# Optimization experiments

Measured on AMD Instinct MI355X. Metric: run time of the kernel, lower is better.

Reference implementation:

```python
import jax, jax.numpy as jnp
import numpy as np

N_NODES = 50000
N_EDGES = 800000
N_GRAPHS = 64
HEADS = 8
HID = 16
D = HEADS * HID  # 128
N_CLASSES = 10
NEG_SLOPE = 0.2
N_LAYERS = 5


def setup_inputs() -> dict:
    key = jax.random.key(0)
    ks = jax.random.split(key, 12)
    x = jax.random.normal(ks[0], (N_NODES, D), dtype=jnp.float32)
    edge_index = jax.random.randint(ks[1], (2, N_EDGES), 0, N_NODES, dtype=jnp.int32)
    batch = jnp.sort(jax.random.randint(ks[2], (N_NODES,), 0, N_GRAPHS, dtype=jnp.int32))
    s = 1.0 / np.sqrt(D)
    # all 5 GATv2 layers share the same shapes (in = 8*hidden = 128); stack on axis 0
    Wl = jax.random.normal(ks[3], (N_LAYERS, D, D), dtype=jnp.float32) * s
    bl = jnp.zeros((N_LAYERS, D), dtype=jnp.float32)
    Wr = jax.random.normal(ks[4], (N_LAYERS, D, D), dtype=jnp.float32) * s
    br = jnp.zeros((N_LAYERS, D), dtype=jnp.float32)
    att = jax.random.normal(ks[5], (N_LAYERS, HEADS, HID), dtype=jnp.float32) * (1.0 / np.sqrt(HID))
    bias = jnp.zeros((N_LAYERS, D), dtype=jnp.float32)
    Wout = jax.random.normal(ks[6], (D, N_CLASSES), dtype=jnp.float32) * s
    bout = jnp.zeros((N_CLASSES,), dtype=jnp.float32)
    return {"x": x, "edge_index": edge_index, "batch": batch,
            "Wl": Wl, "bl": bl, "Wr": Wr, "br": br, "att": att, "bias": bias,
            "Wout": Wout, "bout": bout}


def gatv2_layer(x, src, dst, Wl, bl, Wr, br, att, bias):
    # x: [N, D_in]; returns [N, HEADS*HID]
    n = x.shape[0]
    xl = (x @ Wl + bl).reshape(n, HEADS, HID)   # source/message transform
    xr = (x @ Wr + br).reshape(n, HEADS, HID)   # target transform
    # GATv2 attention: att . leaky_relu(xl_j + xr_i) per edge, per head
    e = jax.nn.leaky_relu(xl[src] + xr[dst], NEG_SLOPE)          # [E, H, C]
    logits = jnp.einsum('ehc,hc->eh', e, att)                    # [E, H]
    # segment-softmax over incoming edges of each dst node
    m = jax.ops.segment_max(logits, dst, num_segments=n)         # [N, H]
    p = jnp.exp(logits - m[dst])
    denom = jax.ops.segment_sum(p, dst, num_segments=n)          # [N, H]
    alpha = p / denom[dst]                                       # [E, H]
    msg = xl[src] * alpha[:, :, None]                            # [E, H, C]
    out = jax.ops.segment_sum(msg, dst, num_segments=n)
    return out.reshape(n, HEADS * HID) + bias


def reference(x, edge_index, batch, Wl, bl, Wr, br, att, bias, Wout, bout):
    n = x.shape[0]
    # GATv2Conv(add_self_loops=True): append self loops to the edge list
    loops = jnp.arange(n, dtype=edge_index.dtype)
    src = jnp.concatenate([edge_index[0], loops])
    dst = jnp.concatenate([edge_index[1], loops])
    h = x
    for l in range(N_LAYERS):
        h = gatv2_layer(h, src, dst, Wl[l], bl[l], Wr[l], br[l], att[l], bias[l])
        h = jax.nn.elu(h)
    # global mean pool over graphs
    sums = jax.ops.segment_sum(h, batch, num_segments=N_GRAPHS)       # [G, D]
    counts = jax.ops.segment_sum(jnp.ones((n,), h.dtype), batch, num_segments=N_GRAPHS)
    pooled = sums / jnp.maximum(counts, 1.0)[:, None]
    logits = pooled @ Wout + bout
    return jax.nn.log_softmax(logits, axis=1)
```

## Files before the change

kernel.cpp:

```cpp
#include <hip/hip_runtime.h>
#include <hip/hip_bf16.h>
#include <math.h>

#define DD 128
#define HEADS 8
#define HID 16
#define NEG_SLOPE 0.2f
#define N_LAYERS 5
#define N_GRAPHS 64
#define N_CLASSES 10
#define NBINS 256
#define BIN_CAP 8192

typedef __bf16 bf16x8 __attribute__((ext_vector_type(8)));
typedef float f32x4 __attribute__((ext_vector_type(4)));

__device__ __forceinline__ float bflo(unsigned u) { return __uint_as_float(u << 16); }
__device__ __forceinline__ float bfhi(unsigned u) { return __uint_as_float(u & 0xffff0000u); }
__device__ __forceinline__ float bf1(unsigned short us) { return __uint_as_float(((unsigned)us) << 16); }
__device__ __forceinline__ unsigned short f2bf(float f) {
    unsigned u = __float_as_uint(f);
    u += 0x7fffu + ((u >> 16) & 1u);
    return (unsigned short)(u >> 16);
}
__device__ __forceinline__ unsigned pack2bf(float a, float b) {
    return (unsigned)f2bf(a) | ((unsigned)f2bf(b) << 16);
}

#define WCNT (N_LAYERS * 4 * 16 * 64)


__global__ void k_setup(const float* __restrict__ x, unsigned* __restrict__ xb,
                        const float* __restrict__ Wl, const float* __restrict__ Wr,
                        unsigned short* __restrict__ wB,
                        float* __restrict__ pooled, float* __restrict__ counts, int n2) {
    int id = blockIdx.x * 256 + threadIdx.x;
    if (id < n2) {
        float2 v = *(const float2*)(x + 2 * (size_t)id);
        xb[id] = pack2bf(v.x, v.y);
        return;
    }
    id -= n2;
    if (id < WCNT) {
        int lane = id & 63;
        int ntg  = (id >> 6) & 15;
        int ks   = (id >> 10) & 3;
        int l    = id >> 12;
        int q = lane >> 4, r = lane & 15;
        int n = ntg * 16 + r;
        const float* W = ((n < DD) ? Wl : Wr) + (size_t)l * DD * DD;
        int nn = n & (DD - 1);
        size_t off = (size_t)l * (4 * 16 * 64 * 8) + ((size_t)(ks * 16 + ntg) * 64 + lane) * 8;
        for (int j = 0; j < 8; ++j) {
            int k = ks * 32 + q * 8 + j;
            wB[off + j] = f2bf(W[(size_t)k * DD + nn]);
        }
        return;
    }
    id -= WCNT;
    if (id < N_GRAPHS * DD) { pooled[id] = 0.f; return; }
    id -= N_GRAPHS * DD;
    if (id < N_GRAPHS) counts[id] = 0.f;
}


__global__ __launch_bounds__(256) void k_bin_cnt(const int* __restrict__ ei,
        int* __restrict__ cnt, int n_edges, int n_total, int chunk,
        unsigned long long bin_mul) {
    __shared__ int hist[NBINS];
    int tid = threadIdx.x;
    hist[tid] = 0;
    __syncthreads();
    int beg = blockIdx.x * chunk;
    int end = beg + chunk; if (end > n_total) end = n_total;
    for (int e = beg + tid; e < end; e += 256) {
        int d = (e < n_edges) ? ei[n_edges + e] : (e - n_edges);
        int b = (int)(((unsigned long long)(unsigned)d * bin_mul) >> 32);
        atomicAdd(&hist[b], 1);
    }
    __syncthreads();
    cnt[tid * 256 + blockIdx.x] = hist[tid];
}

__global__ __launch_bounds__(256) void k_bin_scan(int* __restrict__ cnt, int* __restrict__ btot) {
    __shared__ int wsum[4];
    int b = blockIdx.x, t = threadIdx.x, wv = t >> 6, ln = t & 63;
    int v = cnt[b * 256 + t];
    int x = v;
#pragma unroll
    for (int ofs = 1; ofs < 64; ofs <<= 1) {
        int tt = __shfl_up(x, ofs);
        if (ln >= ofs) x += tt;
    }
    if (ln == 63) wsum[wv] = x;
    __syncthreads();
    int off = 0;
    for (int k = 0; k < wv; k++) off += wsum[k];
    int incl = off + x;
    cnt[b * 256 + t] = incl - v;
    if (t == 255) btot[b] = incl;
}

__global__ __launch_bounds__(256) void k_tot_scan(const int* __restrict__ btot,
        int* __restrict__ bin_start, int* __restrict__ row_ptr, int n_nodes) {
    __shared__ int wsum[4];
    int t = threadIdx.x, wv = t >> 6, ln = t & 63;
    int v = btot[t];
    int x = v;
#pragma unroll
    for (int ofs = 1; ofs < 64; ofs <<= 1) {
        int tt = __shfl_up(x, ofs);
        if (ln >= ofs) x += tt;
    }
    if (ln == 63) wsum[wv] = x;
    __syncthreads();
    int off = 0;
    for (int k = 0; k < wv; k++) off += wsum[k];
    int incl = off + x;
    bin_start[t] = incl - v;
    if (t == 255) { bin_start[256] = incl; row_ptr[n_nodes] = incl; }
}

__global__ __launch_bounds__(256) void k_bin_scatter(const int* __restrict__ ei,
        const int* __restrict__ cnt, const int* __restrict__ bin_start,
        unsigned* __restrict__ binned, int n_edges, int n_total, int chunk,
        unsigned long long bin_mul) {
    __shared__ int cur[NBINS];
    int tid = threadIdx.x;
    cur[tid] = bin_start[tid] + cnt[tid * 256 + blockIdx.x];
    __syncthreads();
    int beg = blockIdx.x * chunk;
    int end = beg + chunk; if (end > n_total) end = n_total;
    for (int e = beg + tid; e < end; e += 256) {
        int s, d;
        if (e < n_edges) { s = ei[e]; d = ei[n_edges + e]; }
        else { s = d = e - n_edges; }
        int b = (int)(((unsigned long long)(unsigned)d * bin_mul) >> 32);
        int pos = atomicAdd(&cur[b], 1);
        binned[pos] = (unsigned)s | ((unsigned)d << 16);
    }
}

__global__ __launch_bounds__(256) void k_bin_csr(const unsigned* __restrict__ binned,
        const int* __restrict__ bin_start, int* __restrict__ csr_src,
        int* __restrict__ row_ptr, int n_nodes, unsigned long long bin_mul) {
    __shared__ int sbuf[BIN_CAP];
    __shared__ int ldeg[256];
    __shared__ int wsum[4];
    int b = blockIdx.x, t = threadIdx.x, wv = t >> 6, ln = t & 63;
    int lo = (int)(((((unsigned long long)b) << 32) + bin_mul - 1) / bin_mul);
    int hi = (int)(((((unsigned long long)(b + 1)) << 32) + bin_mul - 1) / bin_mul);
    if (hi > n_nodes) hi = n_nodes;
    int estart = bin_start[b], eend = bin_start[b + 1];
    int ne = eend - estart;
    ldeg[t] = 0;
    __syncthreads();
    for (int k = t; k < ne; k += 256) {
        unsigned v = binned[estart + k];
        atomicAdd(&ldeg[(int)(v >> 16) - lo], 1);
    }
    __syncthreads();
    int vdeg = ldeg[t];
    int x = vdeg;
#pragma unroll
    for (int ofs = 1; ofs < 64; ofs <<= 1) {
        int tt = __shfl_up(x, ofs);
        if (ln >= ofs) x += tt;
    }
    if (ln == 63) wsum[wv] = x;
    __syncthreads();
    int off = 0;
    for (int k = 0; k < wv; k++) off += wsum[k];
    int excl = off + x - vdeg;
    if (lo + t < hi) row_ptr[lo + t] = estart + excl;
    ldeg[t] = excl;
    __syncthreads();
    for (int k = t; k < ne; k += 256) {
        unsigned v = binned[estart + k];
        int pos = atomicAdd(&ldeg[(int)(v >> 16) - lo], 1);
        sbuf[pos] = (int)(v & 0xffffu);
    }
    __syncthreads();
    for (int k = t; k < ne; k += 256)
        csr_src[estart + k] = sbuf[k];
}


__global__ __launch_bounds__(256) void k_gemm_mfma(
    const unsigned short* __restrict__ in, const unsigned short* __restrict__ wB,
    const float* __restrict__ bl, const float* __restrict__ br,
    unsigned short* __restrict__ xl, unsigned short* __restrict__ xr, int n_nodes) {
    int w = threadIdx.x >> 6;
    int lane = threadIdx.x & 63;
    int q = lane >> 4, r = lane & 15;
    int blk = blockIdx.x;

    f32x4 acc[4][4] = {};
#pragma unroll
    for (int ks = 0; ks < 4; ++ks) {
        bf16x8 bh[4];
#pragma unroll
        for (int nt = 0; nt < 4; ++nt) {
            int ntg = w * 4 + nt;
            bh[nt] = *(const bf16x8*)(wB + ((size_t)(ks * 16 + ntg) * 64 + lane) * 8);
        }
        bf16x8 ah[4];
#pragma unroll
        for (int mt = 0; mt < 4; ++mt) {
            int node = blk * 64 + mt * 16 + r;
            if (node >= n_nodes) node = n_nodes - 1;
            ah[mt] = *(const bf16x8*)(in + (size_t)node * DD + ks * 32 + q * 8);
        }
#pragma unroll
        for (int mt = 0; mt < 4; ++mt)
#pragma unroll
            for (int nt = 0; nt < 4; ++nt)
                acc[mt][nt] = __builtin_amdgcn_mfma_f32_16x16x32_bf16(ah[mt], bh[nt], acc[mt][nt], 0, 0, 0);
    }
#pragma unroll
    for (int nt = 0; nt < 4; ++nt) {
        int col = w * 64 + nt * 16 + r;
        float bv = (col < DD) ? bl[col] : br[col - DD];
        unsigned short* dstbase = (col < DD) ? (xl + col) : (xr + (col - DD));
#pragma unroll
        for (int mt = 0; mt < 4; ++mt)
#pragma unroll
            for (int reg = 0; reg < 4; ++reg) {
                int node = blk * 64 + mt * 16 + q * 4 + reg;
                if (node < n_nodes)
                    dstbase[(size_t)node * DD] = f2bf(acc[mt][nt][reg] + bv);
            }
    }
}


__global__ __launch_bounds__(256) void k_node_agg(
    const unsigned short* __restrict__ xl, const unsigned short* __restrict__ xr,
    const int* __restrict__ row_ptr, const int* __restrict__ csr_src,
    const float* __restrict__ att, const float* __restrict__ bias,
    unsigned short* __restrict__ h_out, int n_nodes) {
    int wave = threadIdx.x >> 6;
    int lane = threadIdx.x & 63;
    int node = blockIdx.x * 4 + wave;
    if (node >= n_nodes) return;
    int grp = lane >> 4, sl = lane & 15;
    int beg = row_ptr[node], end = row_ptr[node + 1];

    uint4 xru = *(const uint4*)(xr + (size_t)node * DD + sl * 8);
    float xr0 = bflo(xru.x), xr1 = bfhi(xru.x), xr2 = bflo(xru.y), xr3 = bfhi(xru.y);
    float xr4 = bflo(xru.z), xr5 = bfhi(xru.z), xr6 = bflo(xru.w), xr7 = bfhi(xru.w);
    float4 at0 = *(const float4*)(att + sl * 8);
    float4 at1 = *(const float4*)(att + sl * 8 + 4);

    float l = 0.f;
    float a0 = 0.f, a1 = 0.f, a2 = 0.f, a3 = 0.f, a4 = 0.f, a5 = 0.f, a6 = 0.f, a7 = 0.f;

    int t0 = beg + grp;
    uint4 xu = make_uint4(0u, 0u, 0u, 0u);
    int sidx = 0;
    if (t0 < end) {
        int s = csr_src[t0];
        xu = *(const uint4*)(xl + (size_t)s * DD + sl * 8);
    }
    if (t0 + 4 < end) sidx = csr_src[t0 + 4];

    for (int t = t0; t < end; t += 4) {
        uint4 cur = xu;
        int snew = 0;
        if (t + 8 < end) snew = csr_src[t + 8];
        if (t + 4 < end) xu = *(const uint4*)(xl + (size_t)sidx * DD + sl * 8);
        sidx = snew;

        float x0 = bflo(cur.x), x1 = bfhi(cur.x), x2 = bflo(cur.y), x3 = bfhi(cur.y);
        float x4 = bflo(cur.z), x5 = bfhi(cur.z), x6 = bflo(cur.w), x7 = bfhi(cur.w);
        float v0 = x0 + xr0; v0 = v0 > 0.f ? v0 : NEG_SLOPE * v0;
        float v1 = x1 + xr1; v1 = v1 > 0.f ? v1 : NEG_SLOPE * v1;
        float v2 = x2 + xr2; v2 = v2 > 0.f ? v2 : NEG_SLOPE * v2;
        float v3 = x3 + xr3; v3 = v3 > 0.f ? v3 : NEG_SLOPE * v3;
        float v4 = x4 + xr4; v4 = v4 > 0.f ? v4 : NEG_SLOPE * v4;
        float v5 = x5 + xr5; v5 = v5 > 0.f ? v5 : NEG_SLOPE * v5;
        float v6 = x6 + xr6; v6 = v6 > 0.f ? v6 : NEG_SLOPE * v6;
        float v7 = x7 + xr7; v7 = v7 > 0.f ? v7 : NEG_SLOPE * v7;
        float lg = at0.x * v0 + at0.y * v1 + at0.z * v2 + at0.w * v3 +
                   at1.x * v4 + at1.y * v5 + at1.z * v6 + at1.w * v7;
        lg += __shfl_xor(lg, 1);
        float p = __expf(lg);
        l += p;
        a0 += p * x0; a1 += p * x1; a2 += p * x2; a3 += p * x3;
        a4 += p * x4; a5 += p * x5; a6 += p * x6; a7 += p * x7;
    }
    l  += __shfl_xor(l, 16);  l  += __shfl_xor(l, 32);
    a0 += __shfl_xor(a0, 16); a0 += __shfl_xor(a0, 32);
    a1 += __shfl_xor(a1, 16); a1 += __shfl_xor(a1, 32);
    a2 += __shfl_xor(a2, 16); a2 += __shfl_xor(a2, 32);
    a3 += __shfl_xor(a3, 16); a3 += __shfl_xor(a3, 32);
    a4 += __shfl_xor(a4, 16); a4 += __shfl_xor(a4, 32);
    a5 += __shfl_xor(a5, 16); a5 += __shfl_xor(a5, 32);
    a6 += __shfl_xor(a6, 16); a6 += __shfl_xor(a6, 32);
    a7 += __shfl_xor(a7, 16); a7 += __shfl_xor(a7, 32);

    if (grp == 0) {
        float4 bv0 = *(const float4*)(bias + sl * 8);
        float4 bv1 = *(const float4*)(bias + sl * 8 + 4);
        float rl = 1.f / l;
        float o0 = a0 * rl + bv0.x; o0 = o0 > 0.f ? o0 : __expf(o0) - 1.f;
        float o1 = a1 * rl + bv0.y; o1 = o1 > 0.f ? o1 : __expf(o1) - 1.f;
        float o2 = a2 * rl + bv0.z; o2 = o2 > 0.f ? o2 : __expf(o2) - 1.f;
        float o3 = a3 * rl + bv0.w; o3 = o3 > 0.f ? o3 : __expf(o3) - 1.f;
        float o4 = a4 * rl + bv1.x; o4 = o4 > 0.f ? o4 : __expf(o4) - 1.f;
        float o5 = a5 * rl + bv1.y; o5 = o5 > 0.f ? o5 : __expf(o5) - 1.f;
        float o6 = a6 * rl + bv1.z; o6 = o6 > 0.f ? o6 : __expf(o6) - 1.f;
        float o7 = a7 * rl + bv1.w; o7 = o7 > 0.f ? o7 : __expf(o7) - 1.f;
        uint4 o;
        o.x = pack2bf(o0, o1); o.y = pack2bf(o2, o3);
        o.z = pack2bf(o4, o5); o.w = pack2bf(o6, o7);
        *(uint4*)(h_out + (size_t)node * DD + sl * 8) = o;
    }
}


__global__ void k_pool2(const unsigned short* __restrict__ h, const int* __restrict__ batch,
                        float* __restrict__ pooled, float* __restrict__ counts,
                        int n_nodes, int chunk) {
    int c = threadIdx.x;
    int beg = blockIdx.x * chunk;
    if (beg >= n_nodes) return;
    int end = beg + chunk; if (end > n_nodes) end = n_nodes;
    int cur = batch[beg];
    float acc = 0.f; int cnt = 0;
    for (int node = beg; node < end; ++node) {
        int g = batch[node];
        if (g != cur) {
            atomicAdd(&pooled[cur * DD + c], acc);
            if (c == 0) atomicAdd(&counts[cur], (float)cnt);
            acc = 0.f; cnt = 0; cur = g;
        }
        acc += bf1(h[(size_t)node * DD + c]);
        cnt++;
    }
    atomicAdd(&pooled[cur * DD + c], acc);
    if (c == 0) atomicAdd(&counts[cur], (float)cnt);
}

__global__ void k_final(const float* __restrict__ pooled, const float* __restrict__ counts,
                        const float* __restrict__ Wout, const float* __restrict__ bout,
                        float* __restrict__ out) {
    __shared__ float slog[N_GRAPHS * N_CLASSES];
    int t = threadIdx.x;
    int g = t / N_CLASSES, c = t % N_CLASSES;
    float cnt = fmaxf(counts[g], 1.f);
    float acc = bout[c];
    for (int k = 0; k < DD; k++)
        acc += (pooled[g * DD + k] / cnt) * Wout[k * N_CLASSES + c];
    slog[t] = acc;
    __syncthreads();
    float mx = -INFINITY;
    for (int j = 0; j < N_CLASSES; j++) mx = fmaxf(mx, slog[g * N_CLASSES + j]);
    float se = 0.f;
    for (int j = 0; j < N_CLASSES; j++) se += __expf(slog[g * N_CLASSES + j] - mx);
    out[t] = acc - mx - __logf(se);
}

extern "C" void kernel_launch(void* const* d_in, const int* in_sizes, int n_in,
                              void* d_out, int out_size, void* d_ws, size_t ws_size,
                              hipStream_t stream) {
    const float* x     = (const float*)d_in[0];
    const int*   ei    = (const int*)d_in[1];
    const int*   batch = (const int*)d_in[2];
    const float* Wl    = (const float*)d_in[3];
    const float* bl    = (const float*)d_in[4];
    const float* Wr    = (const float*)d_in[5];
    const float* br    = (const float*)d_in[6];
    const float* att   = (const float*)d_in[7];
    const float* bias  = (const float*)d_in[8];
    const float* Wout  = (const float*)d_in[9];
    const float* bout  = (const float*)d_in[10];
    float* out = (float*)d_out;

    int n_nodes = in_sizes[0] / DD;
    int n_edges = in_sizes[1] / 2;
    int n_total = n_edges + n_nodes;
    int ND = n_nodes * DD;

    const int WPL = 4 * 16 * 64 * 8;
    unsigned long long bin_mul = (((unsigned long long)NBINS) << 32) / (unsigned)n_nodes;

    unsigned short* hb  = (unsigned short*)d_ws;
    unsigned short* xb  = hb + (size_t)ND;
    unsigned short* xlb = xb + (size_t)ND;
    unsigned short* xrb = xlb + (size_t)ND;
    unsigned short* wB  = xrb + (size_t)ND;
    int*      cnt       = (int*)(wB + (size_t)N_LAYERS * WPL);
    int*      btot      = cnt + NBINS * 256;
    int*      bin_start = btot + NBINS;
    unsigned* binned    = (unsigned*)(bin_start + NBINS + 1);
    int*      csr_src   = (int*)(binned + n_total);
    int*      row_ptr   = csr_src + n_total;
    float*    pooled    = (float*)(row_ptr + n_nodes + 1);
    float*    counts    = pooled + N_GRAPHS * DD;

    dim3 b256(256);
    int gGemm = (n_nodes + 63) / 64;
    int gAgg  = (n_nodes + 3) / 4;
    int chunk = (n_total + 255) / 256;
    int poolBlocks = 1024;
    int poolChunk = (n_nodes + poolBlocks - 1) / poolBlocks;

    int n2 = ND / 2;
    int setupTotal = n2 + WCNT + N_GRAPHS * DD + N_GRAPHS;
    k_setup<<<(setupTotal + 255) / 256, b256, 0, stream>>>(x, (unsigned*)xb, Wl, Wr, wB,
                                                           pooled, counts, n2);
    k_bin_cnt<<<256, b256, 0, stream>>>(ei, cnt, n_edges, n_total, chunk, bin_mul);
    k_bin_scan<<<NBINS, b256, 0, stream>>>(cnt, btot);
    k_tot_scan<<<1, b256, 0, stream>>>(btot, bin_start, row_ptr, n_nodes);
    k_bin_scatter<<<256, b256, 0, stream>>>(ei, cnt, bin_start, binned, n_edges, n_total,
                                            chunk, bin_mul);
    k_bin_csr<<<NBINS, b256, 0, stream>>>(binned, bin_start, csr_src, row_ptr, n_nodes, bin_mul);

    for (int l = 0; l < N_LAYERS; l++) {
        const float* bl_l   = bl   + (size_t)l * DD;
        const float* br_l   = br   + (size_t)l * DD;
        const float* att_l  = att  + (size_t)l * HEADS * HID;
        const float* bias_l = bias + (size_t)l * DD;
        const unsigned short* in = (l == 0) ? xb : hb;

        k_gemm_mfma<<<gGemm, b256, 0, stream>>>(in, wB + (size_t)l * WPL, bl_l, br_l,
                                                xlb, xrb, n_nodes);
        k_node_agg<<<gAgg, b256, 0, stream>>>(xlb, xrb, row_ptr, csr_src, att_l, bias_l, hb, n_nodes);
    }

    k_pool2<<<poolBlocks, dim3(128), 0, stream>>>(hb, batch, pooled, counts, n_nodes, poolChunk);
    k_final<<<1, dim3(N_GRAPHS * N_CLASSES), 0, stream>>>(pooled, counts, Wout, bout, out);
}
```

Measured before the change: 498.3 us.

## Fuse CSR build and pooling stages into persistent kernels with grid barriers

Merges setup, binning count, scans, scatter and CSR build into one 256-block kernel that separates phases with atomic-counter grid barriers, and merges pooling with the final classifier the same way. This cuts the per-launch overhead and inter-kernel gaps of roughly eight small launches. The leaky-relu also becomes a branchless fmaxf. The cost is a memset for the barrier counters. Correctness also depends on all 256 blocks being co-resident and on setup work being grid-strided over 256 blocks, which may reduce parallelism for the conversion step.

```diff
diff --git a/kernel.cpp b/kernel.cpp
--- a/kernel.cpp
+++ b/kernel.cpp
@@ -29,160 +29,169 @@
 
 #define WCNT (N_LAYERS * 4 * 16 * 64)
 
-
-__global__ void k_setup(const float* __restrict__ x, unsigned* __restrict__ xb,
-                        const float* __restrict__ Wl, const float* __restrict__ Wr,
-                        unsigned short* __restrict__ wB,
-                        float* __restrict__ pooled, float* __restrict__ counts, int n2) {
-    int id = blockIdx.x * 256 + threadIdx.x;
-    if (id < n2) {
-        float2 v = *(const float2*)(x + 2 * (size_t)id);
-        xb[id] = pack2bf(v.x, v.y);
-        return;
-    }
-    id -= n2;
-    if (id < WCNT) {
-        int lane = id & 63;
-        int ntg  = (id >> 6) & 15;
-        int ks   = (id >> 10) & 3;
-        int l    = id >> 12;
-        int q = lane >> 4, r = lane & 15;
-        int n = ntg * 16 + r;
-        const float* W = ((n < DD) ? Wl : Wr) + (size_t)l * DD * DD;
-        int nn = n & (DD - 1);
-        size_t off = (size_t)l * (4 * 16 * 64 * 8) + ((size_t)(ks * 16 + ntg) * 64 + lane) * 8;
-        for (int j = 0; j < 8; ++j) {
-            int k = ks * 32 + q * 8 + j;
-            wB[off + j] = f2bf(W[(size_t)k * DD + nn]);
-        }
-        return;
-    }
-    id -= WCNT;
-    if (id < N_GRAPHS * DD) { pooled[id] = 0.f; return; }
-    id -= N_GRAPHS * DD;
-    if (id < N_GRAPHS) counts[id] = 0.f;
-}
-
-
-__global__ __launch_bounds__(256) void k_bin_cnt(const int* __restrict__ ei,
-        int* __restrict__ cnt, int n_edges, int n_total, int chunk,
-        unsigned long long bin_mul) {
-    __shared__ int hist[NBINS];
-    int tid = threadIdx.x;
-    hist[tid] = 0;
+__device__ __forceinline__ void gbar(int* cnt, int target) {
     __syncthreads();
-    int beg = blockIdx.x * chunk;
-    int end = beg + chunk; if (end > n_total) end = n_total;
-    for (int e = beg + tid; e < end; e += 256) {
-        int d = (e < n_edges) ? ei[n_edges + e] : (e - n_edges);
-        int b = (int)(((unsigned long long)(unsigned)d * bin_mul) >> 32);
-        atomicAdd(&hist[b], 1);
+    if (threadIdx.x == 0) {
+        __threadfence();
+        atomicAdd(cnt, 1);
+        while (atomicAdd(cnt, 0) < target) { }
+        __threadfence();
     }
     __syncthreads();
-    cnt[tid * 256 + blockIdx.x] = hist[tid];
-}
-
-__global__ __launch_bounds__(256) void k_bin_scan(int* __restrict__ cnt, int* __restrict__ btot) {
-    __shared__ int wsum[4];
-    int b = blockIdx.x, t = threadIdx.x, wv = t >> 6, ln = t & 63;
-    int v = cnt[b * 256 + t];
-    int x = v;
-#pragma unroll
-    for (int ofs = 1; ofs < 64; ofs <<= 1) {
-        int tt = __shfl_up(x, ofs);
-        if (ln >= ofs) x += tt;
-    }
-    if (ln == 63) wsum[wv] = x;
+}
+
+
+__global__ __launch_bounds__(256) void k_prep(
+        const float* __restrict__ x, unsigned* __restrict__ xb,
+        const float* __restrict__ Wl, const float* __restrict__ Wr,
+        unsigned short* __restrict__ wB, float* __restrict__ pooled,
+        float* __restrict__ counts, const int* __restrict__ ei,
+        int* __restrict__ cnt, int* __restrict__ btot, int* __restrict__ bin_start,
+        unsigned* __restrict__ binned, int* __restrict__ csr_src, int* __restrict__ row_ptr,
+        int* __restrict__ bar, int n2, int n_nodes, int n_edges, int n_total,
+        int chunk, unsigned long long bin_mul) {
+    __shared__ int smem[BIN_CAP];
+    __shared__ int saux[256];
+    __shared__ int swsum[4];
+    int t = threadIdx.x, blk = blockIdx.x;
+    int wv = t >> 6, ln = t & 63;
+
+    int setupTotal = n2 + WCNT + N_GRAPHS * DD + N_GRAPHS;
+    for (int id = blk * 256 + t; id < setupTotal; id += 256 * 256) {
+        int i = id;
+        if (i < n2) {
+            float2 v = *(const float2*)(x + 2 * (size_t)i);
+            xb[i] = pack2bf(v.x, v.y);
+            continue;
+        }
+        i -= n2;
+        if (i < WCNT) {
+            int lane = i & 63;
+            int ntg  = (i >> 6) & 15;
+            int ks   = (i >> 10) & 3;
+            int l    = i >> 12;
+            int q = lane >> 4, r = lane & 15;
+            int n = ntg * 16 + r;
+            const float* W = ((n < DD) ? Wl : Wr) + (size_t)l * DD * DD;
+            int nn = n & (DD - 1);
+            size_t off = (size_t)l * (4 * 16 * 64 * 8) + ((size_t)(ks * 16 + ntg) * 64 + lane) * 8;
+            for (int j = 0; j < 8; ++j) {
+                int k = ks * 32 + q * 8 + j;
+                wB[off + j] = f2bf(W[(size_t)k * DD + nn]);
+            }
+            continue;
+        }
+        i -= WCNT;
+        if (i < N_GRAPHS * DD) { pooled[i] = 0.f; continue; }
+        i -= N_GRAPHS * DD;
+        counts[i] = 0.f;
+    }
+    saux[t] = 0;
     __syncthreads();
-    int off = 0;
-    for (int k = 0; k < wv; k++) off += wsum[k];
-    int incl = off + x;
-    cnt[b * 256 + t] = incl - v;
-    if (t == 255) btot[b] = incl;
-}
-
-__global__ __launch_bounds__(256) void k_tot_scan(const int* __restrict__ btot,
-        int* __restrict__ bin_start, int* __restrict__ row_ptr, int n_nodes) {
-    __shared__ int wsum[4];
-    int t = threadIdx.x, wv = t >> 6, ln = t & 63;
-    int v = btot[t];
-    int x = v;
-#pragma unroll
-    for (int ofs = 1; ofs < 64; ofs <<= 1) {
-        int tt = __shfl_up(x, ofs);
-        if (ln >= ofs) x += tt;
-    }
-    if (ln == 63) wsum[wv] = x;
+    {
+        int beg = blk * chunk;
+        int end = beg + chunk; if (end > n_total) end = n_total;
+        for (int e = beg + t; e < end; e += 256) {
+            int d = (e < n_edges) ? ei[n_edges + e] : (e - n_edges);
+            int b = (int)(((unsigned long long)(unsigned)d * bin_mul) >> 32);
+            atomicAdd(&saux[b], 1);
+        }
+    }
     __syncthreads();
-    int off = 0;
-    for (int k = 0; k < wv; k++) off += wsum[k];
-    int incl = off + x;
-    bin_start[t] = incl - v;
-    if (t == 255) { bin_start[256] = incl; row_ptr[n_nodes] = incl; }
-}
-
-__global__ __launch_bounds__(256) void k_bin_scatter(const int* __restrict__ ei,
-        const int* __restrict__ cnt, const int* __restrict__ bin_start,
-        unsigned* __restrict__ binned, int n_edges, int n_total, int chunk,
-        unsigned long long bin_mul) {
-    __shared__ int cur[NBINS];
-    int tid = threadIdx.x;
-    cur[tid] = bin_start[tid] + cnt[tid * 256 + blockIdx.x];
+    cnt[t * 256 + blk] = saux[t];
+    gbar(bar, 256);
+
+    {
+        int v = cnt[blk * 256 + t];
+        int xx = v;
+#pragma unroll
+        for (int ofs = 1; ofs < 64; ofs <<= 1) {
+            int tt = __shfl_up(xx, ofs);
+            if (ln >= ofs) xx += tt;
+        }
+        if (ln == 63) swsum[wv] = xx;
+        __syncthreads();
+        int off = 0;
+        for (int k = 0; k < wv; k++) off += swsum[k];
+        int incl = off + xx;
+        cnt[blk * 256 + t] = incl - v;
+        if (t == 255) btot[blk] = incl;
+    }
+    gbar(bar, 512);
+
+    if (blk == 0) {
+        int v = btot[t];
+        int xx = v;
+#pragma unroll
+        for (int ofs = 1; ofs < 64; ofs <<= 1) {
+            int tt = __shfl_up(xx, ofs);
+            if (ln >= ofs) xx += tt;
+        }
+        if (ln == 63) swsum[wv] = xx;
+        __syncthreads();
+        int off = 0;
+        for (int k = 0; k < wv; k++) off += swsum[k];
+        int incl = off + xx;
+        bin_start[t] = incl - v;
+        if (t == 255) { bin_start[256] = incl; row_ptr[n_nodes] = incl; }
+    }
+    gbar(bar, 768);
+
+    saux[t] = bin_start[t] + cnt[t * 256 + blk];
     __syncthreads();
-    int beg = blockIdx.x * chunk;
-    int end = beg + chunk; if (end > n_total) end = n_total;
-    for (int e = beg + tid; e < end; e += 256) {
-        int s, d;
-        if (e < n_edges) { s = ei[e]; d = ei[n_edges + e]; }
-        else { s = d = e - n_edges; }
-        int b = (int)(((unsigned long long)(unsigned)d * bin_mul) >> 32);
-        int pos = atomicAdd(&cur[b], 1);
-        binned[pos] = (unsigned)s | ((unsigned)d << 16);
-    }
-}
-
-__global__ __launch_bounds__(256) void k_bin_csr(const unsigned* __restrict__ binned,
-        const int* __restrict__ bin_start, int* __restrict__ csr_src,
-        int* __restrict__ row_ptr, int n_nodes, unsigned long long bin_mul) {
-    __shared__ int sbuf[BIN_CAP];
-    __shared__ int ldeg[256];
-    __shared__ int wsum[4];
-    int b = blockIdx.x, t = threadIdx.x, wv = t >> 6, ln = t & 63;
-    int lo = (int)(((((unsigned long long)b) << 32) + bin_mul - 1) / bin_mul);
-    int hi = (int)(((((unsigned long long)(b + 1)) << 32) + bin_mul - 1) / bin_mul);
-    if (hi > n_nodes) hi = n_nodes;
-    int estart = bin_start[b], eend = bin_start[b + 1];
-    int ne = eend - estart;
-    ldeg[t] = 0;
-    __syncthreads();
-    for (int k = t; k < ne; k += 256) {
-        unsigned v = binned[estart + k];
-        atomicAdd(&ldeg[(int)(v >> 16) - lo], 1);
-    }
-    __syncthreads();
-    int vdeg = ldeg[t];
-    int x = vdeg;
-#pragma unroll
-    for (int ofs = 1; ofs < 64; ofs <<= 1) {
-        int tt = __shfl_up(x, ofs);
-        if (ln >= ofs) x += tt;
-    }
-    if (ln == 63) wsum[wv] = x;
-    __syncthreads();
-    int off = 0;
-    for (int k = 0; k < wv; k++) off += wsum[k];
-    int excl = off + x - vdeg;
-    if (lo + t < hi) row_ptr[lo + t] = estart + excl;
-    ldeg[t] = excl;
-    __syncthreads();
-    for (int k = t; k < ne; k += 256) {
-        unsigned v = binned[estart + k];
-        int pos = atomicAdd(&ldeg[(int)(v >> 16) - lo], 1);
-        sbuf[pos] = (int)(v & 0xffffu);
-    }
-    __syncthreads();
-    for (int k = t; k < ne; k += 256)
-        csr_src[estart + k] = sbuf[k];
+    {
+        int beg = blk * chunk;
+        int end = beg + chunk; if (end > n_total) end = n_total;
+        for (int e = beg + t; e < end; e += 256) {
+            int s, d;
+            if (e < n_edges) { s = ei[e]; d = ei[n_edges + e]; }
+            else { s = d = e - n_edges; }
+            int b = (int)(((unsigned long long)(unsigned)d * bin_mul) >> 32);
+            int pos = atomicAdd(&saux[b], 1);
+            binned[pos] = (unsigned)s | ((unsigned)d << 16);
+        }
+    }
+    gbar(bar, 1024);
+
+    {
+        int b = blk;
+        int lo = (int)(((((unsigned long long)b) << 32) + bin_mul - 1) / bin_mul);
+        int hi = (int)(((((unsigned long long)(b + 1)) << 32) + bin_mul - 1) / bin_mul);
+        if (hi > n_nodes) hi = n_nodes;
+        int estart = bin_start[b], eend = bin_start[b + 1];
+        int ne = eend - estart;
+        saux[t] = 0;
+        __syncthreads();
+        for (int k = t; k < ne; k += 256) {
+            unsigned v = binned[estart + k];
+            atomicAdd(&saux[(int)(v >> 16) - lo], 1);
+        }
+        __syncthreads();
+        int vdeg = saux[t];
+        int xx = vdeg;
+#pragma unroll
+        for (int ofs = 1; ofs < 64; ofs <<= 1) {
+            int tt = __shfl_up(xx, ofs);
+            if (ln >= ofs) xx += tt;
+        }
+        if (ln == 63) swsum[wv] = xx;
+        __syncthreads();
+        int off = 0;
+        for (int k = 0; k < wv; k++) off += swsum[k];
+        int excl = off + xx - vdeg;
+        if (lo + t < hi) row_ptr[lo + t] = estart + excl;
+        __syncthreads();
+        saux[t] = excl;
+        __syncthreads();
+        for (int k = t; k < ne; k += 256) {
+            unsigned v = binned[estart + k];
+            int pos = atomicAdd(&saux[(int)(v >> 16) - lo], 1);
+            smem[pos] = (int)(v & 0xffffu);
+        }
+        __syncthreads();
+        for (int k = t; k < ne; k += 256)
+            csr_src[estart + k] = smem[k];
+    }
 }
 
 
@@ -273,14 +282,14 @@
 
         float x0 = bflo(cur.x), x1 = bfhi(cur.x), x2 = bflo(cur.y), x3 = bfhi(cur.y);
         float x4 = bflo(cur.z), x5 = bfhi(cur.z), x6 = bflo(cur.w), x7 = bfhi(cur.w);
-        float v0 = x0 + xr0; v0 = v0 > 0.f ? v0 : NEG_SLOPE * v0;
-        float v1 = x1 + xr1; v1 = v1 > 0.f ? v1 : NEG_SLOPE * v1;
-        float v2 = x2 + xr2; v2 = v2 > 0.f ? v2 : NEG_SLOPE * v2;
-        float v3 = x3 + xr3; v3 = v3 > 0.f ? v3 : NEG_SLOPE * v3;
-        float v4 = x4 + xr4; v4 = v4 > 0.f ? v4 : NEG_SLOPE * v4;
-        float v5 = x5 + xr5; v5 = v5 > 0.f ? v5 : NEG_SLOPE * v5;
-        float v6 = x6 + xr6; v6 = v6 > 0.f ? v6 : NEG_SLOPE * v6;
-        float v7 = x7 + xr7; v7 = v7 > 0.f ? v7 : NEG_SLOPE * v7;
+        float v0 = x0 + xr0; v0 = fmaxf(v0, NEG_SLOPE * v0);
+        float v1 = x1 + xr1; v1 = fmaxf(v1, NEG_SLOPE * v1);
+        float v2 = x2 + xr2; v2 = fmaxf(v2, NEG_SLOPE * v2);
+        float v3 = x3 + xr3; v3 = fmaxf(v3, NEG_SLOPE * v3);
+        float v4 = x4 + xr4; v4 = fmaxf(v4, NEG_SLOPE * v4);
+        float v5 = x5 + xr5; v5 = fmaxf(v5, NEG_SLOPE * v5);
+        float v6 = x6 + xr6; v6 = fmaxf(v6, NEG_SLOPE * v6);
+        float v7 = x7 + xr7; v7 = fmaxf(v7, NEG_SLOPE * v7);
         float lg = at0.x * v0 + at0.y * v1 + at0.z * v2 + at0.w * v3 +
                    at1.x * v4 + at1.y * v5 + at1.z * v6 + at1.w * v7;
         lg += __shfl_xor(lg, 1);
@@ -319,46 +328,52 @@
 }
 
 
-__global__ void k_pool2(const unsigned short* __restrict__ h, const int* __restrict__ batch,
-                        float* __restrict__ pooled, float* __restrict__ counts,
-                        int n_nodes, int chunk) {
+__global__ __launch_bounds__(128) void k_pool_final(
+        const unsigned short* __restrict__ h, const int* __restrict__ batch,
+        float* __restrict__ pooled, float* __restrict__ counts,
+        const float* __restrict__ Wout, const float* __restrict__ bout,
+        float* __restrict__ out, int* __restrict__ bar, int n_nodes, int chunk) {
     int c = threadIdx.x;
     int beg = blockIdx.x * chunk;
-    if (beg >= n_nodes) return;
-    int end = beg + chunk; if (end > n_nodes) end = n_nodes;
-    int cur = batch[beg];
-    float acc = 0.f; int cnt = 0;
-    for (int node = beg; node < end; ++node) {
-        int g = batch[node];
-        if (g != cur) {
-            atomicAdd(&pooled[cur * DD + c], acc);
-            if (c == 0) atomicAdd(&counts[cur], (float)cnt);
-            acc = 0.f; cnt = 0; cur = g;
-        }
-        acc += bf1(h[(size_t)node * DD + c]);
-        cnt++;
-    }
-    atomicAdd(&pooled[cur * DD + c], acc);
-    if (c == 0) atomicAdd(&counts[cur], (float)cnt);
-}
-
-__global__ void k_final(const float* __restrict__ pooled, const float* __restrict__ counts,
-                        const float* __restrict__ Wout, const float* __restrict__ bout,
-                        float* __restrict__ out) {
-    __shared__ float slog[N_GRAPHS * N_CLASSES];
-    int t = threadIdx.x;
-    int g = t / N_CLASSES, c = t % N_CLASSES;
-    float cnt = fmaxf(counts[g], 1.f);
-    float acc = bout[c];
-    for (int k = 0; k < DD; k++)
-        acc += (pooled[g * DD + k] / cnt) * Wout[k * N_CLASSES + c];
-    slog[t] = acc;
-    __syncthreads();
-    float mx = -INFINITY;
-    for (int j = 0; j < N_CLASSES; j++) mx = fmaxf(mx, slog[g * N_CLASSES + j]);
-    float se = 0.f;
-    for (int j = 0; j < N_CLASSES; j++) se += __expf(slog[g * N_CLASSES + j] - mx);
-    out[t] = acc - mx - __logf(se);
+    if (beg < n_nodes) {
+        int end = beg + chunk; if (end > n_nodes) end = n_nodes;
+        int cur = batch[beg];
+        float acc = 0.f; int cnt = 0;
+        for (int node = beg; node < end; ++node) {
+            int g = batch[node];
+            if (g != cur) {
+                atomicAdd(&pooled[cur * DD + c], acc);
+                if (c == 0) atomicAdd(&counts[cur], (float)cnt);
+                acc = 0.f; cnt = 0; cur = g;
+            }
+            acc += bf1(h[(size_t)node * DD + c]);
+            cnt++;
+        }
+        atomicAdd(&pooled[cur * DD + c], acc);
+        if (c == 0) atomicAdd(&counts[cur], (float)cnt);
+    }
+    gbar(bar, 256);
+    if (blockIdx.x == 0) {
+        __shared__ float slog[N_GRAPHS * N_CLASSES];
+        for (int i = c; i < N_GRAPHS * N_CLASSES; i += 128) {
+            int g = i / N_CLASSES, cl = i % N_CLASSES;
+            float cntv = fmaxf(counts[g], 1.f);
+            float acc = bout[cl];
+            for (int k = 0; k < DD; k++)
+                acc += (pooled[g * DD + k] / cntv) * Wout[k * N_CLASSES + cl];
+            slog[i] = acc;
+        }
+        __syncthreads();
+        for (int g = c; g < N_GRAPHS; g += 128) {
+            float mx = -INFINITY;
+            for (int j = 0; j < N_CLASSES; j++) mx = fmaxf(mx, slog[g * N_CLASSES + j]);
+            float se = 0.f;
+            for (int j = 0; j < N_CLASSES; j++) se += __expf(slog[g * N_CLASSES + j] - mx);
+            float lse = mx + __logf(se);
+            for (int j = 0; j < N_CLASSES; j++)
+                out[g * N_CLASSES + j] = slog[g * N_CLASSES + j] - lse;
+        }
+    }
 }
 
 extern "C" void kernel_launch(void* const* d_in, const int* in_sizes, int n_in,
@@ -385,7 +400,8 @@
     const int WPL = 4 * 16 * 64 * 8;
     unsigned long long bin_mul = (((unsigned long long)NBINS) << 32) / (unsigned)n_nodes;
 
-    unsigned short* hb  = (unsigned short*)d_ws;
+    int* bar            = (int*)d_ws;
+    unsigned short* hb  = (unsigned short*)((char*)d_ws + 256);
     unsigned short* xb  = hb + (size_t)ND;
     unsigned short* xlb = xb + (size_t)ND;
     unsigned short* xrb = xlb + (size_t)ND;
@@ -403,19 +419,13 @@
     int gGemm = (n_nodes + 63) / 64;
     int gAgg  = (n_nodes + 3) / 4;
     int chunk = (n_total + 255) / 256;
-    int poolBlocks = 1024;
-    int poolChunk = (n_nodes + poolBlocks - 1) / poolBlocks;
-
+    int poolChunk = (n_nodes + 255) / 256;
     int n2 = ND / 2;
-    int setupTotal = n2 + WCNT + N_GRAPHS * DD + N_GRAPHS;
-    k_setup<<<(setupTotal + 255) / 256, b256, 0, stream>>>(x, (unsigned*)xb, Wl, Wr, wB,
-                                                           pooled, counts, n2);
-    k_bin_cnt<<<256, b256, 0, stream>>>(ei, cnt, n_edges, n_total, chunk, bin_mul);
-    k_bin_scan<<<NBINS, b256, 0, stream>>>(cnt, btot);
-    k_tot_scan<<<1, b256, 0, stream>>>(btot, bin_start, row_ptr, n_nodes);
-    k_bin_scatter<<<256, b256, 0, stream>>>(ei, cnt, bin_start, binned, n_edges, n_total,
-                                            chunk, bin_mul);
-    k_bin_csr<<<NBINS, b256, 0, stream>>>(binned, bin_start, csr_src, row_ptr, n_nodes, bin_mul);
+
+    hipMemsetAsync(d_ws, 0, 256, stream);
+    k_prep<<<256, b256, 0, stream>>>(x, (unsigned*)xb, Wl, Wr, wB, pooled, counts, ei,
+                                     cnt, btot, bin_start, binned, csr_src, row_ptr,
+                                     &bar[0], n2, n_nodes, n_edges, n_total, chunk, bin_mul);
 
     for (int l = 0; l < N_LAYERS; l++) {
         const float* bl_l   = bl   + (size_t)l * DD;
@@ -429,6 +439,6 @@
         k_node_agg<<<gAgg, b256, 0, stream>>>(xlb, xrb, row_ptr, csr_src, att_l, bias_l, hb, n_nodes);
     }
 
-    k_pool2<<<poolBlocks, dim3(128), 0, stream>>>(hb, batch, pooled, counts, n_nodes, poolChunk);
-    k_final<<<1, dim3(N_GRAPHS * N_CLASSES), 0, stream>>>(pooled, counts, Wout, bout, out);
-}
+    k_pool_final<<<256, dim3(128), 0, stream>>>(hb, batch, pooled, counts, Wout, bout,
+                                                out, &bar[1], n_nodes, poolChunk);
+}
```

New measurement: 662.0 us. 1.33x slower.
